# Optimization experiments

Hardware: AMD Instinct MI355X
Metric: run time of the kernel (lower is better)

## Reference

```python
import jax, jax.numpy as jnp
import numpy as np

B, SEQ, D_IN = 1, 2048, 2048
NUM_HEADS, DIM_HEAD, NUM_KV = 32, 128, 8
GROUP = NUM_HEADS // NUM_KV
EPS = 1e-6
ROPE_BASE = 1000000.0  # Qwen3 rope theta


def setup_inputs() -> dict:
    key = jax.random.key(0)
    ks = jax.random.split(key, 6)
    x = jax.random.normal(ks[0], (B, SEQ, D_IN), jnp.float32)
    Wq = jax.random.normal(ks[1], (D_IN, NUM_HEADS * DIM_HEAD), jnp.float32) * 0.02
    Wk = jax.random.normal(ks[2], (D_IN, NUM_KV * DIM_HEAD), jnp.float32) * 0.02
    Wv = jax.random.normal(ks[3], (D_IN, NUM_KV * DIM_HEAD), jnp.float32) * 0.02
    Wo = jax.random.normal(ks[4], (NUM_HEADS * DIM_HEAD, D_IN), jnp.float32) * 0.02
    q_scale = jnp.ones((DIM_HEAD,), jnp.float32)
    k_scale = jnp.ones((DIM_HEAD,), jnp.float32)
    # RoPE tables: angles for half dims, duplicated to full head dim (rotate-half convention)
    inv_freq = 1.0 / (ROPE_BASE ** (jnp.arange(0, DIM_HEAD, 2, dtype=jnp.float32) / DIM_HEAD))
    pos = jnp.arange(SEQ, dtype=jnp.float32)
    angles = pos[:, None] * inv_freq[None, :]              # [SEQ, DIM_HEAD//2]
    angles = jnp.concatenate([angles, angles], axis=-1)    # [SEQ, DIM_HEAD]
    cos = jnp.cos(angles)
    sin = jnp.sin(angles)
    mask = jnp.triu(jnp.ones((SEQ, SEQ), dtype=bool), k=1)  # True = masked (causal)
    return {"x": x, "Wq": Wq, "Wk": Wk, "Wv": Wv, "Wo": Wo,
            "q_scale": q_scale, "k_scale": k_scale,
            "cos": cos, "sin": sin, "mask": mask, "start_pos": 0}


def _rmsnorm(h, scale):
    var = jnp.mean(h * h, axis=-1, keepdims=True)
    return h * jax.lax.rsqrt(var + EPS) * scale


def _rope(h, cos, sin, offset):
    # h: [b, heads, n, d]; rotate-half RoPE
    n = h.shape[2]
    c = cos[offset:offset + n][None, None]  # [1,1,n,d]
    s = sin[offset:offset + n][None, None]
    half = h.shape[-1] // 2
    h1, h2 = h[..., :half], h[..., half:]
    rotated = jnp.concatenate([-h2, h1], axis=-1)
    return h * c + rotated * s


def reference(x, Wq, Wk, Wv, Wo, q_scale, k_scale, cos, sin, mask, start_pos):
    b, n, _ = x.shape
    q = (x @ Wq).reshape(b, n, NUM_HEADS, DIM_HEAD).transpose(0, 2, 1, 3)  # [b,H,n,d]
    k = (x @ Wk).reshape(b, n, NUM_KV, DIM_HEAD).transpose(0, 2, 1, 3)     # [b,K,n,d]
    v = (x @ Wv).reshape(b, n, NUM_KV, DIM_HEAD).transpose(0, 2, 1, 3)
    q = _rmsnorm(q, q_scale)
    k = _rmsnorm(k, k_scale)
    q = _rope(q, cos, sin, start_pos)
    k = _rope(k, cos, sin, start_pos)
    # next_cache = (k, v); no prior cache (prefill)
    # GQA: group query heads per kv head instead of repeat_interleave on K/V
    qg = q.reshape(b, NUM_KV, GROUP, n, DIM_HEAD)
    scores = jnp.einsum('bkgqd,bknd->bkgqn', qg, k)
    scores = jnp.where(mask[:n, :n], -jnp.inf, scores)
    weights = jax.nn.softmax(scores / jnp.sqrt(jnp.float32(DIM_HEAD)), axis=-1)
    ctx = jnp.einsum('bkgqn,bknd->bkgqd', weights, v)
    ctx = ctx.reshape(b, NUM_HEADS, n, DIM_HEAD).transpose(0, 2, 1, 3).reshape(b, n, NUM_HEADS * DIM_HEAD)
    out = ctx @ Wo
    return (out, k, v)
```

## Files before the change

kernel.cpp:

```cpp
#include <hip/hip_runtime.h>
#include <hip/hip_bf16.h>
#include <cstdint>

typedef unsigned short u16;
typedef __bf16 bf16x8 __attribute__((ext_vector_type(8)));
typedef float f32x4 __attribute__((ext_vector_type(4)));

#define ASYNC16(g, l)                                                                   \
  __builtin_amdgcn_global_load_lds((__attribute__((address_space(1))) const void*)(g),  \
                                   (__attribute__((address_space(3))) void*)(l), 16, 0, 0)

static __device__ __forceinline__ u16 f2bf(float f) {
  unsigned u = __float_as_uint(f);
  u += 0x7FFFu + ((u >> 16) & 1u);
  return (u16)(u >> 16);
}

static __device__ __forceinline__ float fexp2(float x) {
#if __has_builtin(__builtin_amdgcn_exp2f)
  return __builtin_amdgcn_exp2f(x);
#else
  return exp2f(x);
#endif
}

__global__ __launch_bounds__(256) void cast_bf16(const float* __restrict__ src,
                                                 u16* __restrict__ dst, int n8) {
  int i = blockIdx.x * 256 + threadIdx.x;
  if (i >= n8) return;
  const float4* s4 = (const float4*)src;
  float4 a = s4[2 * (size_t)i], b = s4[2 * (size_t)i + 1];
  u16 r[8] = {f2bf(a.x), f2bf(a.y), f2bf(a.z), f2bf(a.w),
              f2bf(b.x), f2bf(b.y), f2bf(b.z), f2bf(b.w)};
  *(uint4*)(dst + 8 * (size_t)i) = *(uint4*)r;
}

__global__ __launch_bounds__(256) void tcast(const float* __restrict__ src, int ld_src, int col0,
                                             int rows, int cols, u16* __restrict__ dst, int ld_dst) {
  __shared__ float tile[32][33];
  int z = blockIdx.z;
  const float* s = src + col0 + (size_t)z * cols;
  u16* d = dst + (size_t)z * cols * ld_dst;
  int cb = blockIdx.x * 32, rb = blockIdx.y * 32;
  int tx = threadIdx.x, ty = threadIdx.y;
#pragma unroll
  for (int i = 0; i < 4; ++i) {
    int r = rb + ty + i * 8;
    tile[ty + i * 8][tx] = s[(size_t)r * ld_src + cb + tx];
  }
  __syncthreads();
#pragma unroll
  for (int i = 0; i < 4; ++i) {
    int c = cb + ty + i * 8;
    d[(size_t)c * ld_dst + rb + tx] = f2bf(tile[tx][ty + i * 8]);
  }
}

__global__ __launch_bounds__(256) void tcast_v(const float* __restrict__ QKV,
                                               u16* __restrict__ Vt, float* __restrict__ vout) {
  __shared__ float tile[32][33];
  int kv = blockIdx.z;
  const float* s = QKV + 5120 + (size_t)kv * 128;
  u16* d = Vt + (size_t)kv * 128 * 2048;
  float* vo = vout + (size_t)kv * 2048 * 128;
  int cb = blockIdx.x * 32, rb = blockIdx.y * 32;
  int tx = threadIdx.x, ty = threadIdx.y;
#pragma unroll
  for (int i = 0; i < 4; ++i) {
    int r = rb + ty + i * 8;
    float val = s[(size_t)r * 6144 + cb + tx];
    tile[ty + i * 8][tx] = val;
    vo[(size_t)r * 128 + cb + tx] = val;
  }
  __syncthreads();
#pragma unroll
  for (int i = 0; i < 4; ++i) {
    int c = cb + ty + i * 8;
    d[(size_t)c * 2048 + rb + tx] = f2bf(tile[tx][ty + i * 8]);
  }
}

__global__ __launch_bounds__(256) void gemm_bt(const u16* __restrict__ A, const u16* __restrict__ Bt,
                                               float* __restrict__ C, int M, int N, int K) {
  __shared__ char smem[32768];
  const int t = threadIdx.x;
  const int w = t >> 6, l = t & 63, la = l & 15, lh = l >> 4;
  const int wr = w >> 1, wc = w & 1;
  const int m0 = blockIdx.y * 128, n0 = blockIdx.x * 128;
  const int z = blockIdx.z;
  const int kLen = K / gridDim.z, kBeg = z * kLen;
  C += (size_t)z * M * N;
  const u16* Ab = A + (size_t)m0 * K + (size_t)(t >> 2) * K + (t & 3) * 8 + kBeg;
  const u16* Bb = Bt + (size_t)n0 * K + (size_t)(t >> 2) * K + (t & 3) * 8 + kBeg;
  const size_t rowStep = (size_t)64 * K;
  f32x4 acc[4][4];
#pragma unroll
  for (int m = 0; m < 4; ++m)
#pragma unroll
    for (int n = 0; n < 4; ++n) acc[m][n] = (f32x4){0.f, 0.f, 0.f, 0.f};

  auto STAGE = [&](int buf, int k0) {
    char* As = smem + buf * 16384;
    char* Bs = As + 8192;
    ASYNC16(Ab + k0, As + w * 1024);
    ASYNC16(Ab + rowStep + k0, As + 4096 + w * 1024);
    ASYNC16(Bb + k0, Bs + w * 1024);
    ASYNC16(Bb + rowStep + k0, Bs + 4096 + w * 1024);
  };

  STAGE(0, 0);
  asm volatile("s_waitcnt vmcnt(0)" ::: "memory");
  __builtin_amdgcn_s_barrier();
  __builtin_amdgcn_sched_barrier(0);

  const int nIt = kLen / 32;
  int buf = 0;
  for (int it = 0; it < nIt; ++it) {
    if (it + 1 < nIt) STAGE(buf ^ 1, (it + 1) * 32);
    char* As = smem + buf * 16384;
    char* Bs = As + 8192;
    bf16x8 af[4], bg[4];
#pragma unroll
    for (int m = 0; m < 4; ++m)
      af[m] = *(const bf16x8*)(As + ((wr * 64 + m * 16 + la) * 32 + lh * 8) * 2);
#pragma unroll
    for (int n = 0; n < 4; ++n)
      bg[n] = *(const bf16x8*)(Bs + ((wc * 64 + n * 16 + la) * 32 + lh * 8) * 2);
#pragma unroll
    for (int m = 0; m < 4; ++m)
#pragma unroll
      for (int n = 0; n < 4; ++n)
        acc[m][n] = __builtin_amdgcn_mfma_f32_16x16x32_bf16(af[m], bg[n], acc[m][n], 0, 0, 0);
    asm volatile("s_waitcnt vmcnt(0)" ::: "memory");
    __builtin_amdgcn_s_barrier();
    __builtin_amdgcn_sched_barrier(0);
    buf ^= 1;
  }
#pragma unroll
  for (int m = 0; m < 4; ++m)
#pragma unroll
    for (int n = 0; n < 4; ++n) {
      int row = m0 + wr * 64 + m * 16 + lh * 4;
      int col = n0 + wc * 64 + n * 16 + la;
      float* cp = C + (size_t)row * N + col;
#pragma unroll
      for (int r = 0; r < 4; ++r) cp[(size_t)r * N] = acc[m][n][r];
    }
}

__global__ __launch_bounds__(256) void addf(const float* __restrict__ a, const float* __restrict__ b,
                                            float* __restrict__ o, int n4) {
  int i = blockIdx.x * 256 + threadIdx.x;
  if (i >= n4) return;
  float4 x = ((const float4*)a)[i];
  float4 y = ((const float4*)b)[i];
  float4 r = {x.x + y.x, x.y + y.y, x.z + y.z, x.w + y.w};
  ((float4*)o)[i] = r;
}

__global__ __launch_bounds__(256) void qk_norm_rope(const float* __restrict__ QKV,
                                                    const float* __restrict__ q_scale,
                                                    const float* __restrict__ k_scale,
                                                    const float* __restrict__ cosT,
                                                    const float* __restrict__ sinT,
                                                    u16* __restrict__ Qb, u16* __restrict__ Kb,
                                                    float* __restrict__ kout) {
  int w = threadIdx.x >> 6, d = threadIdx.x & 63;
  int sidx = blockIdx.x * 4 + w, hi = blockIdx.y;
  bool isQ = hi < 32;
  int col = isQ ? hi * 128 : 4096 + (hi - 32) * 128;
  const float* row = QKV + (size_t)sidx * 6144 + col;
  float v1 = row[d], v2 = row[d + 64];
  float ss = v1 * v1 + v2 * v2;
#pragma unroll
  for (int off = 32; off; off >>= 1) ss += __shfl_xor(ss, off);
  float rn = rsqrtf(ss * (1.0f / 128.0f) + 1e-6f);
  const float* sc = isQ ? q_scale : k_scale;
  float n1 = v1 * rn * sc[d], n2 = v2 * rn * sc[d + 64];
  float c1 = cosT[sidx * 128 + d], s1 = sinT[sidx * 128 + d];
  float c2 = cosT[sidx * 128 + d + 64], s2 = sinT[sidx * 128 + d + 64];
  float o1 = n1 * c1 - n2 * s1;
  float o2 = n2 * c2 + n1 * s2;
  if (isQ) {
    const float qs = 0.12751878878561148f;
    u16* dst = Qb + ((size_t)hi * 2048 + sidx) * 128;
    dst[d] = f2bf(o1 * qs);
    dst[d + 64] = f2bf(o2 * qs);
  } else {
    int kvh = hi - 32;
    u16* dst = Kb + ((size_t)kvh * 2048 + sidx) * 128;
    dst[d] = f2bf(o1);
    dst[d + 64] = f2bf(o2);
    float* fo = kout + ((size_t)kvh * 2048 + sidx) * 128;
    fo[d] = o1;
    fo[d + 64] = o2;
  }
}

__global__ __launch_bounds__(256) void attn(const u16* __restrict__ Q, const u16* __restrict__ Kb,
                                            const u16* __restrict__ Vt, u16* __restrict__ ctx) {
  extern __shared__ char smem[];
  char* Ps = smem + 65536;
  const int t = threadIdx.x, w = t >> 6, l = t & 63, la = l & 15, lh = l >> 4;
  const int bid = blockIdx.x;
  const int g = bid & 7, j_ = bid >> 3;
  const int h = g * 4 + (j_ & 3), p_ = j_ >> 2;
  const int kv = g;
  const int qhA = p_, qhB = 31 - p_;
  const int ntA = qhA + 1, ntT = 33;
  const u16* Kh = Kb + (size_t)kv * 2048 * 128;
  const u16* Vh = Vt + (size_t)kv * 128 * 2048;
  const int keyS = t >> 4, pgK = t & 15;
  const int dS = t >> 3, pgV = t & 7;

  bf16x8 aq[4];
  f32x4 o[8];
  float rmax[4], rsum[4];

  auto loadQ = [&](int q0_) {
    const u16* Qh = Q + ((size_t)h * 2048 + q0_ + w * 16) * 128;
#pragma unroll
    for (int ks = 0; ks < 4; ++ks)
      aq[ks] = *(const bf16x8*)(Qh + la * 128 + ks * 32 + lh * 8);
  };
  auto resetAcc = [&]() {
#pragma unroll
    for (int n = 0; n < 8; ++n) o[n] = (f32x4){0.f, 0.f, 0.f, 0.f};
#pragma unroll
    for (int r = 0; r < 4; ++r) { rmax[r] = -INFINITY; rsum[r] = 0.f; }
  };
  auto STAGE = [&](int buf, int tt) {
    int j0 = (tt >= ntA ? tt - ntA : tt) * 64;
    char* Kd = smem + buf * 32768;
    char* Vd = Kd + 16384;
#pragma unroll
    for (int i = 0; i < 4; ++i) {
      int key = i * 16 + keyS;
      int lg = pgK ^ (key & 7);
      ASYNC16(Kh + (size_t)(j0 + key) * 128 + lg * 8, Kd + i * 4096 + w * 1024);
    }
#pragma unroll
    for (int i = 0; i < 4; ++i) {
      int d = i * 32 + dS;
      int lg = pgV ^ (d & 7);
      ASYNC16(Vh + (size_t)d * 2048 + j0 + lg * 8, Vd + i * 4096 + w * 1024);
    }
  };
  auto epilogue = [&](int q0_) {
#pragma unroll
    for (int r = 0; r < 4; ++r) {
      float inv = 1.f / rsum[r];
      int row = q0_ + w * 16 + lh * 4 + r;
      u16* dst = ctx + (size_t)row * 4096 + h * 128;
#pragma unroll
      for (int n = 0; n < 8; ++n) dst[n * 16 + la] = f2bf(o[n][r] * inv);
    }
  };

  int q0 = qhA * 64;
  loadQ(q0);
  resetAcc();
  STAGE(0, 0);
  asm volatile("s_waitcnt vmcnt(0)" ::: "memory");
  __builtin_amdgcn_s_barrier();
  __builtin_amdgcn_sched_barrier(0);

  int cur = 0;
  for (int tt = 0; tt < ntT; ++tt) {
    if (tt + 1 < ntT) STAGE(cur ^ 1, tt + 1);
    if (tt == ntA) {
      epilogue(q0);
      q0 = qhB * 64;
      loadQ(q0);
      resetAcc();
    }
    const int j0 = (tt >= ntA ? tt - ntA : tt) * 64;
    char* Ks = smem + cur * 32768;
    char* Vs = Ks + 16384;
    f32x4 s[4];
#pragma unroll
    for (int n = 0; n < 4; ++n) s[n] = (f32x4){0.f, 0.f, 0.f, 0.f};
    __builtin_amdgcn_s_setprio(1);
#pragma unroll
    for (int ks = 0; ks < 4; ++ks) {
      bf16x8 bk[4];
#pragma unroll
      for (int n = 0; n < 4; ++n) {
        int key = n * 16 + la;
        int lg = (ks * 4 + lh) ^ (key & 7);
        bk[n] = *(const bf16x8*)(Ks + key * 256 + lg * 16);
      }
#pragma unroll
      for (int n = 0; n < 4; ++n)
        s[n] = __builtin_amdgcn_mfma_f32_16x16x32_bf16(aq[ks], bk[n], s[n], 0, 0, 0);
    }
    __builtin_amdgcn_s_setprio(0);
    {
      int qmin = q0 + w * 16;
#pragma unroll
      for (int n = 0; n < 4; ++n) {
        int jb = j0 + n * 16;
        if (jb + 15 > qmin) {
          int j = jb + la;
#pragma unroll
          for (int r = 0; r < 4; ++r) {
            int q = qmin + lh * 4 + r;
            if (j > q) s[n][r] = -INFINITY;
          }
        }
      }
    }
    float tm[4];
    bool need = false;
#pragma unroll
    for (int r = 0; r < 4; ++r) {
      float v = fmaxf(fmaxf(s[0][r], s[1][r]), fmaxf(s[2][r], s[3][r]));
      v = fmaxf(v, __shfl_xor(v, 1));
      v = fmaxf(v, __shfl_xor(v, 2));
      v = fmaxf(v, __shfl_xor(v, 4));
      v = fmaxf(v, __shfl_xor(v, 8));
      tm[r] = v;
      need |= (v > rmax[r]);
    }
    if (__any(need)) {
#pragma unroll
      for (int r = 0; r < 4; ++r) {
        float nm = fmaxf(rmax[r], tm[r]);
        float fac = fexp2(rmax[r] - nm);
        rmax[r] = nm;
        rsum[r] *= fac;
#pragma unroll
        for (int n = 0; n < 8; ++n) o[n][r] *= fac;
      }
    }
#pragma unroll
    for (int r = 0; r < 4; ++r) {
      float nm = rmax[r];
      float p0 = fexp2(s[0][r] - nm);
      float p1 = fexp2(s[1][r] - nm);
      float p2 = fexp2(s[2][r] - nm);
      float p3 = fexp2(s[3][r] - nm);
      float ps = p0 + p1 + p2 + p3;
      ps += __shfl_xor(ps, 1);
      ps += __shfl_xor(ps, 2);
      ps += __shfl_xor(ps, 4);
      ps += __shfl_xor(ps, 8);
      rsum[r] += ps;
      int qloc = w * 16 + lh * 4 + r;
      int sw = qloc & 7;
      u16 pb[4] = {f2bf(p0), f2bf(p1), f2bf(p2), f2bf(p3)};
#pragma unroll
      for (int n = 0; n < 4; ++n) {
        int key = n * 16 + la;
        *(u16*)(Ps + qloc * 128 + ((key >> 3) ^ sw) * 16 + (key & 7) * 2) = pb[n];
      }
    }
#pragma unroll
    for (int kk = 0; kk < 2; ++kk) {
      bf16x8 ap;
      {
        int qloc = w * 16 + la;
        int lg = (kk * 4 + lh) ^ (qloc & 7);
        ap = *(const bf16x8*)(Ps + qloc * 128 + lg * 16);
      }
      __builtin_amdgcn_s_setprio(1);
#pragma unroll
      for (int n = 0; n < 8; ++n) {
        int d = n * 16 + la;
        int lg = (kk * 4 + lh) ^ (d & 7);
        bf16x8 bv = *(const bf16x8*)(Vs + d * 128 + lg * 16);
        o[n] = __builtin_amdgcn_mfma_f32_16x16x32_bf16(ap, bv, o[n], 0, 0, 0);
      }
      __builtin_amdgcn_s_setprio(0);
    }
    asm volatile("s_waitcnt vmcnt(0)" ::: "memory");
    __builtin_amdgcn_s_barrier();
    __builtin_amdgcn_sched_barrier(0);
    cur ^= 1;
  }
  epilogue(q0);
}

extern "C" void kernel_launch(void* const* d_in, const int* in_sizes, int n_in,
                              void* d_out, int out_size, void* d_ws, size_t ws_size,
                              hipStream_t stream) {
  (void)in_sizes; (void)n_in; (void)out_size; (void)ws_size;
  const float* x = (const float*)d_in[0];
  const float* Wq = (const float*)d_in[1];
  const float* Wk = (const float*)d_in[2];
  const float* Wv = (const float*)d_in[3];
  const float* Wo = (const float*)d_in[4];
  const float* q_scale = (const float*)d_in[5];
  const float* k_scale = (const float*)d_in[6];
  const float* cosT = (const float*)d_in[7];
  const float* sinT = (const float*)d_in[8];
  float* out = (float*)d_out;
  float* kout = out + (size_t)4194304;
  float* vout = out + (size_t)6291456;

  char* p = (char*)d_ws;
  u16* xb = (u16*)p;      p += (size_t)2048 * 2048 * 2;
  u16* WqkvT = (u16*)p;   p += (size_t)6144 * 2048 * 2;
  u16* WoT = (u16*)p;     p += (size_t)2048 * 4096 * 2;
  float* QKV = (float*)p; p += (size_t)2048 * 6144 * 4;
  u16* Qb = (u16*)p;      p += (size_t)32 * 2048 * 128 * 2;
  u16* Kb = (u16*)p;      p += (size_t)8 * 2048 * 128 * 2;
  u16* Vtb = (u16*)p;     p += (size_t)8 * 128 * 2048 * 2;
  u16* ctxb = (u16*)p;    p += (size_t)2048 * 4096 * 2;
  float* Cp = (float*)d_ws;

  cast_bf16<<<2048, 256, 0, stream>>>(x, xb, 524288);
  tcast<<<dim3(128, 64, 1), dim3(32, 8, 1), 0, stream>>>(Wq, 4096, 0, 2048, 4096, WqkvT, 2048);
  tcast<<<dim3(32, 64, 1), dim3(32, 8, 1), 0, stream>>>(Wk, 1024, 0, 2048, 1024,
                                                        WqkvT + (size_t)4096 * 2048, 2048);
  tcast<<<dim3(32, 64, 1), dim3(32, 8, 1), 0, stream>>>(Wv, 1024, 0, 2048, 1024,
                                                        WqkvT + (size_t)5120 * 2048, 2048);
  tcast<<<dim3(64, 128, 1), dim3(32, 8, 1), 0, stream>>>(Wo, 2048, 0, 4096, 2048, WoT, 4096);
  gemm_bt<<<dim3(48, 16, 1), 256, 0, stream>>>(xb, WqkvT, QKV, 2048, 6144, 2048);
  qk_norm_rope<<<dim3(512, 40, 1), 256, 0, stream>>>(QKV, q_scale, k_scale, cosT, sinT, Qb, Kb, kout);
  tcast_v<<<dim3(4, 64, 8), dim3(32, 8, 1), 0, stream>>>(QKV, Vtb, vout);
  attn<<<dim3(512, 1, 1), 256, 73728, stream>>>(Qb, Kb, Vtb, ctxb);
  gemm_bt<<<dim3(16, 16, 2), 256, 0, stream>>>(ctxb, WoT, Cp, 2048, 2048, 4096);
  addf<<<4096, 256, 0, stream>>>(Cp, Cp + (size_t)4194304, out, 1048576);
}
```

Measured before the change: 399.8 us.

## Share K/V tiles across GQA heads in attention; triple-buffer GEMM loads

The attention kernel is reorganised so each block handles one 16-row query chunk for all four query heads of a KV group, one head per wave. The K/V tiles staged in LDS are therefore shared across the GQA group instead of being reloaded per head. Key tiles shrink to 32, the grid doubles to 1024 blocks with less shared memory, and causal chunks are ordered for load balance. The GEMM moves from double to triple buffering with a partial vmcnt wait so loads run two stages ahead, at the cost of more LDS per block.

```diff
diff --git a/kernel.cpp b/kernel.cpp
--- a/kernel.cpp
+++ b/kernel.cpp
@@ -82,7 +82,7 @@
 
 __global__ __launch_bounds__(256) void gemm_bt(const u16* __restrict__ A, const u16* __restrict__ Bt,
                                                float* __restrict__ C, int M, int N, int K) {
-  __shared__ char smem[32768];
+  __shared__ char smem[49152];
   const int t = threadIdx.x;
   const int w = t >> 6, l = t & 63, la = l & 15, lh = l >> 4;
   const int wr = w >> 1, wc = w & 1;
@@ -108,15 +108,18 @@
     ASYNC16(Bb + rowStep + k0, Bs + 4096 + w * 1024);
   };
 
+  const int nIt = kLen / 32;
   STAGE(0, 0);
-  asm volatile("s_waitcnt vmcnt(0)" ::: "memory");
-  __builtin_amdgcn_s_barrier();
-  __builtin_amdgcn_sched_barrier(0);
-
-  const int nIt = kLen / 32;
+  STAGE(1, 32);
+
   int buf = 0;
   for (int it = 0; it < nIt; ++it) {
-    if (it + 1 < nIt) STAGE(buf ^ 1, (it + 1) * 32);
+    if (it + 1 < nIt) {
+      asm volatile("s_waitcnt vmcnt(4)" ::: "memory");
+    } else {
+      asm volatile("s_waitcnt vmcnt(0)" ::: "memory");
+    }
+    __builtin_amdgcn_s_barrier();
     char* As = smem + buf * 16384;
     char* Bs = As + 8192;
     bf16x8 af[4], bg[4];
@@ -131,10 +134,8 @@
 #pragma unroll
       for (int n = 0; n < 4; ++n)
         acc[m][n] = __builtin_amdgcn_mfma_f32_16x16x32_bf16(af[m], bg[n], acc[m][n], 0, 0, 0);
-    asm volatile("s_waitcnt vmcnt(0)" ::: "memory");
-    __builtin_amdgcn_s_barrier();
-    __builtin_amdgcn_sched_barrier(0);
-    buf ^= 1;
+    if (it + 2 < nIt) STAGE((buf + 2) % 3, (it + 2) * 32);
+    buf = (buf + 1) % 3;
   }
 #pragma unroll
   for (int m = 0; m < 4; ++m)
@@ -200,111 +201,92 @@
 __global__ __launch_bounds__(256) void attn(const u16* __restrict__ Q, const u16* __restrict__ Kb,
                                             const u16* __restrict__ Vt, u16* __restrict__ ctx) {
   extern __shared__ char smem[];
-  char* Ps = smem + 65536;
   const int t = threadIdx.x, w = t >> 6, l = t & 63, la = l & 15, lh = l >> 4;
+  char* Ps = smem + 32768 + w * 2048;
   const int bid = blockIdx.x;
-  const int g = bid & 7, j_ = bid >> 3;
-  const int h = g * 4 + (j_ & 3), p_ = j_ >> 2;
-  const int kv = g;
-  const int qhA = p_, qhB = 31 - p_;
-  const int ntA = qhA + 1, ntT = 33;
-  const u16* Kh = Kb + (size_t)kv * 2048 * 128;
-  const u16* Vh = Vt + (size_t)kv * 128 * 2048;
+  const int g = bid & 7;
+  const int v = bid >> 3;
+  const int jj = v & 31, quad = v >> 5;
+  int c;
+  if (quad == 0) c = 127 - jj;
+  else if (quad == 1) c = jj;
+  else if (quad == 2) c = 95 - jj;
+  else c = 32 + jj;
+  const int h = g * 4 + w;
+  const int q0 = c * 16;
+  const int nt = (c + 2) >> 1;
+  const u16* Kh = Kb + (size_t)g * 2048 * 128;
+  const u16* Vh = Vt + (size_t)g * 128 * 2048;
   const int keyS = t >> 4, pgK = t & 15;
-  const int dS = t >> 3, pgV = t & 7;
+  const int dS = t >> 2, jV = t & 3;
 
   bf16x8 aq[4];
+  {
+    const u16* Qh = Q + ((size_t)h * 2048 + q0) * 128;
+#pragma unroll
+    for (int ks = 0; ks < 4; ++ks)
+      aq[ks] = *(const bf16x8*)(Qh + la * 128 + ks * 32 + lh * 8);
+  }
   f32x4 o[8];
   float rmax[4], rsum[4];
-
-  auto loadQ = [&](int q0_) {
-    const u16* Qh = Q + ((size_t)h * 2048 + q0_ + w * 16) * 128;
-#pragma unroll
-    for (int ks = 0; ks < 4; ++ks)
-      aq[ks] = *(const bf16x8*)(Qh + la * 128 + ks * 32 + lh * 8);
+#pragma unroll
+  for (int n = 0; n < 8; ++n) o[n] = (f32x4){0.f, 0.f, 0.f, 0.f};
+#pragma unroll
+  for (int r = 0; r < 4; ++r) { rmax[r] = -INFINITY; rsum[r] = 0.f; }
+
+  auto STAGE = [&](int buf, int jt) {
+    int j0 = jt * 32;
+    char* Kd = smem + buf * 16384;
+    char* Vd = Kd + 8192;
+#pragma unroll
+    for (int i = 0; i < 2; ++i) {
+      int key = i * 16 + keyS;
+      ASYNC16(Kh + (size_t)(j0 + key) * 128 + (pgK ^ (key & 7)) * 8, Kd + i * 4096 + w * 1024);
+    }
+#pragma unroll
+    for (int i = 0; i < 2; ++i) {
+      int d = i * 64 + dS;
+      ASYNC16(Vh + (size_t)d * 2048 + j0 + (jV ^ (d & 3)) * 8, Vd + i * 4096 + w * 1024);
+    }
   };
-  auto resetAcc = [&]() {
-#pragma unroll
-    for (int n = 0; n < 8; ++n) o[n] = (f32x4){0.f, 0.f, 0.f, 0.f};
-#pragma unroll
-    for (int r = 0; r < 4; ++r) { rmax[r] = -INFINITY; rsum[r] = 0.f; }
-  };
-  auto STAGE = [&](int buf, int tt) {
-    int j0 = (tt >= ntA ? tt - ntA : tt) * 64;
-    char* Kd = smem + buf * 32768;
-    char* Vd = Kd + 16384;
-#pragma unroll
-    for (int i = 0; i < 4; ++i) {
-      int key = i * 16 + keyS;
-      int lg = pgK ^ (key & 7);
-      ASYNC16(Kh + (size_t)(j0 + key) * 128 + lg * 8, Kd + i * 4096 + w * 1024);
-    }
-#pragma unroll
-    for (int i = 0; i < 4; ++i) {
-      int d = i * 32 + dS;
-      int lg = pgV ^ (d & 7);
-      ASYNC16(Vh + (size_t)d * 2048 + j0 + lg * 8, Vd + i * 4096 + w * 1024);
-    }
-  };
-  auto epilogue = [&](int q0_) {
-#pragma unroll
-    for (int r = 0; r < 4; ++r) {
-      float inv = 1.f / rsum[r];
-      int row = q0_ + w * 16 + lh * 4 + r;
-      u16* dst = ctx + (size_t)row * 4096 + h * 128;
-#pragma unroll
-      for (int n = 0; n < 8; ++n) dst[n * 16 + la] = f2bf(o[n][r] * inv);
-    }
-  };
-
-  int q0 = qhA * 64;
-  loadQ(q0);
-  resetAcc();
+
   STAGE(0, 0);
   asm volatile("s_waitcnt vmcnt(0)" ::: "memory");
   __builtin_amdgcn_s_barrier();
   __builtin_amdgcn_sched_barrier(0);
 
   int cur = 0;
-  for (int tt = 0; tt < ntT; ++tt) {
-    if (tt + 1 < ntT) STAGE(cur ^ 1, tt + 1);
-    if (tt == ntA) {
-      epilogue(q0);
-      q0 = qhB * 64;
-      loadQ(q0);
-      resetAcc();
-    }
-    const int j0 = (tt >= ntA ? tt - ntA : tt) * 64;
-    char* Ks = smem + cur * 32768;
-    char* Vs = Ks + 16384;
-    f32x4 s[4];
-#pragma unroll
-    for (int n = 0; n < 4; ++n) s[n] = (f32x4){0.f, 0.f, 0.f, 0.f};
+  for (int jt = 0; jt < nt; ++jt) {
+    if (jt + 1 < nt) STAGE(cur ^ 1, jt + 1);
+    const int j0 = jt * 32;
+    char* Ks = smem + cur * 16384;
+    char* Vs = Ks + 8192;
+    f32x4 s[2];
+#pragma unroll
+    for (int n = 0; n < 2; ++n) s[n] = (f32x4){0.f, 0.f, 0.f, 0.f};
     __builtin_amdgcn_s_setprio(1);
 #pragma unroll
     for (int ks = 0; ks < 4; ++ks) {
-      bf16x8 bk[4];
-#pragma unroll
-      for (int n = 0; n < 4; ++n) {
+      bf16x8 bk[2];
+#pragma unroll
+      for (int n = 0; n < 2; ++n) {
         int key = n * 16 + la;
-        int lg = (ks * 4 + lh) ^ (key & 7);
-        bk[n] = *(const bf16x8*)(Ks + key * 256 + lg * 16);
+        bk[n] = *(const bf16x8*)(Ks + key * 256 + (((ks * 4 + lh) ^ (key & 7)) * 16));
       }
 #pragma unroll
-      for (int n = 0; n < 4; ++n)
+      for (int n = 0; n < 2; ++n)
         s[n] = __builtin_amdgcn_mfma_f32_16x16x32_bf16(aq[ks], bk[n], s[n], 0, 0, 0);
     }
     __builtin_amdgcn_s_setprio(0);
-    {
-      int qmin = q0 + w * 16;
-#pragma unroll
-      for (int n = 0; n < 4; ++n) {
+    if (j0 + 31 > q0) {
+#pragma unroll
+      for (int n = 0; n < 2; ++n) {
         int jb = j0 + n * 16;
-        if (jb + 15 > qmin) {
+        if (jb + 15 > q0) {
           int j = jb + la;
 #pragma unroll
           for (int r = 0; r < 4; ++r) {
-            int q = qmin + lh * 4 + r;
+            int q = q0 + lh * 4 + r;
             if (j > q) s[n][r] = -INFINITY;
           }
         }
@@ -314,13 +296,13 @@
     bool need = false;
 #pragma unroll
     for (int r = 0; r < 4; ++r) {
-      float v = fmaxf(fmaxf(s[0][r], s[1][r]), fmaxf(s[2][r], s[3][r]));
-      v = fmaxf(v, __shfl_xor(v, 1));
-      v = fmaxf(v, __shfl_xor(v, 2));
-      v = fmaxf(v, __shfl_xor(v, 4));
-      v = fmaxf(v, __shfl_xor(v, 8));
-      tm[r] = v;
-      need |= (v > rmax[r]);
+      float mv = fmaxf(s[0][r], s[1][r]);
+      mv = fmaxf(mv, __shfl_xor(mv, 1));
+      mv = fmaxf(mv, __shfl_xor(mv, 2));
+      mv = fmaxf(mv, __shfl_xor(mv, 4));
+      mv = fmaxf(mv, __shfl_xor(mv, 8));
+      tm[r] = mv;
+      need |= (mv > rmax[r]);
     }
     if (__any(need)) {
 #pragma unroll
@@ -338,47 +320,42 @@
       float nm = rmax[r];
       float p0 = fexp2(s[0][r] - nm);
       float p1 = fexp2(s[1][r] - nm);
-      float p2 = fexp2(s[2][r] - nm);
-      float p3 = fexp2(s[3][r] - nm);
-      float ps = p0 + p1 + p2 + p3;
+      float ps = p0 + p1;
       ps += __shfl_xor(ps, 1);
       ps += __shfl_xor(ps, 2);
       ps += __shfl_xor(ps, 4);
       ps += __shfl_xor(ps, 8);
       rsum[r] += ps;
-      int qloc = w * 16 + lh * 4 + r;
-      int sw = qloc & 7;
-      u16 pb[4] = {f2bf(p0), f2bf(p1), f2bf(p2), f2bf(p3)};
-#pragma unroll
-      for (int n = 0; n < 4; ++n) {
-        int key = n * 16 + la;
-        *(u16*)(Ps + qloc * 128 + ((key >> 3) ^ sw) * 16 + (key & 7) * 2) = pb[n];
+      int ql = lh * 4 + r;
+      u16 pb[2] = {f2bf(p0), f2bf(p1)};
+#pragma unroll
+      for (int n = 0; n < 2; ++n) {
+        int gkey = n * 2 + (la >> 3);
+        *(u16*)(Ps + ql * 64 + ((gkey ^ (ql & 3)) * 16) + (la & 7) * 2) = pb[n];
       }
     }
-#pragma unroll
-    for (int kk = 0; kk < 2; ++kk) {
-      bf16x8 ap;
-      {
-        int qloc = w * 16 + la;
-        int lg = (kk * 4 + lh) ^ (qloc & 7);
-        ap = *(const bf16x8*)(Ps + qloc * 128 + lg * 16);
-      }
-      __builtin_amdgcn_s_setprio(1);
-#pragma unroll
-      for (int n = 0; n < 8; ++n) {
-        int d = n * 16 + la;
-        int lg = (kk * 4 + lh) ^ (d & 7);
-        bf16x8 bv = *(const bf16x8*)(Vs + d * 128 + lg * 16);
-        o[n] = __builtin_amdgcn_mfma_f32_16x16x32_bf16(ap, bv, o[n], 0, 0, 0);
-      }
-      __builtin_amdgcn_s_setprio(0);
-    }
+    bf16x8 ap = *(const bf16x8*)(Ps + la * 64 + ((lh ^ (la & 3)) * 16));
+    __builtin_amdgcn_s_setprio(1);
+#pragma unroll
+    for (int n = 0; n < 8; ++n) {
+      int d = n * 16 + la;
+      bf16x8 bv = *(const bf16x8*)(Vs + d * 64 + ((lh ^ (d & 3)) * 16));
+      o[n] = __builtin_amdgcn_mfma_f32_16x16x32_bf16(ap, bv, o[n], 0, 0, 0);
+    }
+    __builtin_amdgcn_s_setprio(0);
     asm volatile("s_waitcnt vmcnt(0)" ::: "memory");
     __builtin_amdgcn_s_barrier();
     __builtin_amdgcn_sched_barrier(0);
     cur ^= 1;
   }
-  epilogue(q0);
+#pragma unroll
+  for (int r = 0; r < 4; ++r) {
+    float inv = 1.f / rsum[r];
+    int row = q0 + lh * 4 + r;
+    u16* dst = ctx + (size_t)row * 4096 + h * 128;
+#pragma unroll
+    for (int n = 0; n < 8; ++n) dst[n * 16 + la] = f2bf(o[n][r] * inv);
+  }
 }
 
 extern "C" void kernel_launch(void* const* d_in, const int* in_sizes, int n_in,
@@ -419,7 +396,7 @@
   gemm_bt<<<dim3(48, 16, 1), 256, 0, stream>>>(xb, WqkvT, QKV, 2048, 6144, 2048);
   qk_norm_rope<<<dim3(512, 40, 1), 256, 0, stream>>>(QKV, q_scale, k_scale, cosT, sinT, Qb, Kb, kout);
   tcast_v<<<dim3(4, 64, 8), dim3(32, 8, 1), 0, stream>>>(QKV, Vtb, vout);
-  attn<<<dim3(512, 1, 1), 256, 73728, stream>>>(Qb, Kb, Vtb, ctxb);
+  attn<<<dim3(1024, 1, 1), 256, 40960, stream>>>(Qb, Kb, Vtb, ctxb);
   gemm_bt<<<dim3(16, 16, 2), 256, 0, stream>>>(ctxb, WoT, Cp, 2048, 2048, 4096);
   addf<<<4096, 256, 0, stream>>>(Cp, Cp + (size_t)4194304, out, 1048576);
 }
```

After: 415.0 us. +3.8%, slower.
